# Kernel tuning notes

Measured on AMD Instinct MI355X. Metric: run time of the kernel, lower is better.

## Reference

```python
import jax, jax.numpy as jnp
import numpy as np

ETA = 3.0
KCAP = 96
POS_W = 1.2
LAMBDA_CD = 1.0
LAMBDA_P0 = 1.0
STRIDES = (8.0, 16.0, 32.0)


def _level_terms(pred_reg, pred_obj, pred_cls, gt, stride):
    """Vectorized per-level version of the triple python loop.
    pred_reg: [B,6,H,W], pred_obj/pred_cls: [B,1,H,W], gt: [B,Ng,3,2].
    Returns partial sums (reg, obj, cls, pos_count, neg_count)."""
    B, _, H, W = pred_obj.shape
    HW = H * W
    Ng = gt.shape[1]
    ys = (jnp.arange(H, dtype=jnp.float32) + 0.5) * stride
    xs = (jnp.arange(W, dtype=jnp.float32) + 0.5) * stride
    yy, xx = jnp.meshgrid(ys, xs, indexing='ij')
    px = xx.reshape(-1)  # [HW]
    py = yy.reshape(-1)
    P = px[None, None, :]  # [1,1,HW]
    Q = py[None, None, :]
    # triangle vertices, each [B,Ng,1] for broadcasting against HW
    Ax, Ay = gt[:, :, 0, 0:1], gt[:, :, 0, 1:2]
    Bx, By = gt[:, :, 1, 0:1], gt[:, :, 1, 1:2]
    Cx, Cy = gt[:, :, 2, 0:1], gt[:, :, 2, 1:2]

    def sgn(x1, y1, x2, y2, x3, y3):
        return (x1 - x3) * (y2 - y3) - (x2 - x3) * (y1 - y3)

    d1 = sgn(P, Q, Ax, Ay, Bx, By)
    d2 = sgn(P, Q, Bx, By, Cx, Cy)
    d3 = sgn(P, Q, Cx, Cy, Ax, Ay)
    has_neg = (d1 < 0) | (d2 < 0) | (d3 < 0)
    has_pos = (d1 > 0) | (d2 > 0) | (d3 > 0)
    inside = ~(has_neg & has_pos)  # [B,Ng,HW]

    def segd(x1, y1, x2, y2):
        vx, vy = x2 - x1, y2 - y1
        wx, wy = P - x1, Q - y1
        t = jnp.clip((wx * vx + wy * vy) / (vx * vx + vy * vy + 1e-9), 0.0, 1.0)
        dx = P - (x1 + t * vx)
        dy = Q - (y1 + t * vy)
        return jnp.sqrt(dx * dx + dy * dy + 1e-12)

    dist = jnp.minimum(segd(Ax, Ay, Bx, By),
                       jnp.minimum(segd(Bx, By, Cx, Cy), segd(Cx, Cy, Ax, Ay)))
    pos = inside | (dist <= ETA)  # [B,Ng,HW]

    # top-k cap: keep the KCAP positives with smallest boundary distance
    dmask = jnp.where(pos, dist, jnp.inf)
    negd, idx = jax.lax.top_k(-dmask, KCAP)  # [B,Ng,K]
    keep = jnp.isfinite(negd)                # finite <=> was a positive
    bi = jnp.arange(B)[:, None, None]
    gi = jnp.arange(Ng)[None, :, None]
    capped = jnp.zeros((B, Ng, HW), dtype=bool).at[bi, gi, idx].set(keep)
    m = capped.astype(jnp.float32)
    pos_count = m.sum()

    # objectness BCE-with-logits (pos_weight) over the whole map
    obj_t = capped.any(axis=1).astype(jnp.float32)  # [B,HW]
    x = pred_obj.reshape(B, HW)
    obj_loss = (POS_W * obj_t * jax.nn.softplus(-x)
                + (1.0 - obj_t) * jax.nn.softplus(x)).sum()
    neg_count = jnp.float32(B * HW) - obj_t.sum()

    pred_off = pred_reg.transpose(0, 2, 3, 1).reshape(B, HW, 3, 2)
    centers = jnp.stack([px, py], axis=-1)  # [HW,2]
    gt_off = (gt[:, :, None] - centers[None, None, :, None]) / stride  # [B,Ng,HW,3,2]
    p0 = ((pred_off[:, None, :, 0] - gt_off[:, :, :, 0]) ** 2).sum(-1)  # [B,Ng,HW]
    pp = pred_off[:, None, :, 1:, :]  # [B,1,HW,2,2]
    gg = gt_off[:, :, :, 1:, :]       # [B,Ng,HW,2,2]
    d = jnp.sqrt(((pp[..., :, None, :] - gg[..., None, :, :]) ** 2).sum(-1))  # [B,Ng,HW,2,2]
    cd = d.min(-1).sum(-1) + d.min(-2).sum(-1)  # [B,Ng,HW]
    reg = (m * (LAMBDA_P0 * p0 + LAMBDA_CD * cd)).sum()

    # class BCE on positives only, target = 1
    cls = (m * jax.nn.softplus(-pred_cls.reshape(B, 1, HW))).sum()
    return reg, obj_loss, cls, pos_count, neg_count


def setup_inputs() -> dict:
    key = jax.random.key(0)
    ks = jax.random.split(key, 10)
    B, Ng = 16, 32
    shapes = [(128, 128), (64, 64), (32, 32)]
    inp = {}
    i = 0
    for l, (H, W) in enumerate(shapes):
        inp[f'pred_reg{l}'] = jax.random.normal(ks[i], (B, 6, H, W), dtype=jnp.float32); i += 1
        inp[f'pred_obj{l}'] = jax.random.normal(ks[i], (B, 1, H, W), dtype=jnp.float32); i += 1
        inp[f'pred_cls{l}'] = jax.random.normal(ks[i], (B, 1, H, W), dtype=jnp.float32); i += 1
    inp['gt'] = jax.random.uniform(ks[9], (B, Ng, 3, 2), dtype=jnp.float32) * 1024.0
    return inp


def reference(pred_reg0, pred_obj0, pred_cls0,
              pred_reg1, pred_obj1, pred_cls1,
              pred_reg2, pred_obj2, pred_cls2, gt):
    levels = [(pred_reg0, pred_obj0, pred_cls0),
              (pred_reg1, pred_obj1, pred_cls1),
              (pred_reg2, pred_obj2, pred_cls2)]
    reg = obj = cls = pc = nc = jnp.float32(0.0)
    for (pr, po, pcls), s in zip(levels, STRIDES):
        r, o, c, p, n = _level_terms(pr, po, pcls, gt, s)
        reg += r; obj += o; cls += c; pc += p; nc += n
    pos_eps = jnp.maximum(pc, 1.0)
    total = (reg / pos_eps
             + obj / (pos_eps + jnp.maximum(nc, 1.0))
             + cls / pos_eps)
    return total
```

## Files before the change

kernel.cpp:

```cpp
#include <hip/hip_runtime.h>

#define KCAP 96u
#define CAP 6144
#define PBLK 512
#define NTOT 344064
#define NPAIR 1536
#define CELLS_PB 224

__device__ __forceinline__ float softplus_f(float x) {
    return fmaxf(x, 0.0f) + log1pf(expf(-fabsf(x)));
}

__device__ __forceinline__ void tri_pos_dist(
    float px, float py,
    float ax, float ay, float bx, float by, float cx, float cy,
    bool& pos, float& dist)
{
#pragma clang fp contract(off)
    float d1 = (px - bx) * (ay - by) - (ax - bx) * (py - by);
    float d2 = (px - cx) * (by - cy) - (bx - cx) * (py - cy);
    float d3 = (px - ax) * (cy - ay) - (cx - ax) * (py - ay);
    bool has_neg = (d1 < 0.f) | (d2 < 0.f) | (d3 < 0.f);
    bool has_pos = (d1 > 0.f) | (d2 > 0.f) | (d3 > 0.f);
    bool inside = !(has_neg && has_pos);

    float dAB, dBC, dCA;
    {
        float vx = bx - ax, vy = by - ay, wx = px - ax, wy = py - ay;
        float t = (wx*vx + wy*vy) / (vx*vx + vy*vy + 1e-9f);
        t = fminf(fmaxf(t, 0.0f), 1.0f);
        float dx = px - (ax + t*vx), dy = py - (ay + t*vy);
        dAB = sqrtf(dx*dx + dy*dy + 1e-12f);
    }
    {
        float vx = cx - bx, vy = cy - by, wx = px - bx, wy = py - by;
        float t = (wx*vx + wy*vy) / (vx*vx + vy*vy + 1e-9f);
        t = fminf(fmaxf(t, 0.0f), 1.0f);
        float dx = px - (bx + t*vx), dy = py - (by + t*vy);
        dBC = sqrtf(dx*dx + dy*dy + 1e-12f);
    }
    {
        float vx = ax - cx, vy = ay - cy, wx = px - cx, wy = py - cy;
        float t = (wx*vx + wy*vy) / (vx*vx + vy*vy + 1e-9f);
        t = fminf(fmaxf(t, 0.0f), 1.0f);
        float dx = px - (cx + t*vx), dy = py - (cy + t*vy);
        dCA = sqrtf(dx*dx + dy*dy + 1e-12f);
    }
    dist = fminf(dAB, fminf(dBC, dCA));
    pos = inside || (dist <= 3.0f);
}

__device__ __forceinline__ unsigned bbox_cells(const float* gp, int level) {
    int W; float stride;
    if (level == 0)      { W = 128; stride = 8.0f;  }
    else if (level == 1) { W = 64;  stride = 16.0f; }
    else                 { W = 32;  stride = 32.0f; }
    const float inv = 1.0f / stride;
    float ax = gp[0], ay = gp[1], bx = gp[2], by = gp[3], cx = gp[4], cy = gp[5];
    float minx = fminf(ax, fminf(bx, cx)), maxx = fmaxf(ax, fmaxf(bx, cx));
    float miny = fminf(ay, fminf(by, cy)), maxy = fmaxf(ay, fmaxf(by, cy));
    int wlo = max(0,     (int)floorf((minx - 3.0f) * inv - 0.5f) - 1);
    int whi = min(W - 1, (int)ceilf ((maxx + 3.0f) * inv - 0.5f) + 1);
    int hlo = max(0,     (int)floorf((miny - 3.0f) * inv - 0.5f) - 1);
    int hhi = min(W - 1, (int)ceilf ((maxy + 3.0f) * inv - 0.5f) + 1);
    int ncols = max(0, whi - wlo + 1);
    int nrows = hhi - hlo + 1;
    return (nrows > 0) ? (unsigned)(nrows * ncols) : 0u;
}

__global__ __launch_bounds__(1024) void schedule_kernel(
    const float* __restrict__ gt,
    unsigned* __restrict__ objbits,
    unsigned short* __restrict__ perm)
{
    const int t = threadIdx.x;
    for (int i = t; i < 10752; i += 1024) objbits[i] = 0u;

    __shared__ unsigned d[2048];
    #pragma unroll
    for (int s = 0; s < 2; ++s) {
        int i = t + s * 1024;
        unsigned packed = 0u;
        if (i < NPAIR) {
            unsigned nb = bbox_cells(gt + (i & 511) * 6, i >> 9);
            packed = (nb << 11) | (unsigned)i;
        }
        d[i] = packed;
    }
    __syncthreads();
    for (unsigned k = 2; k <= 2048u; k <<= 1) {
        for (unsigned j = k >> 1; j > 0; j >>= 1) {
            #pragma unroll
            for (int s = 0; s < 2; ++s) {
                int i = t + s * 1024;
                int ixj = i ^ (int)j;
                if (ixj > i) {
                    unsigned a = d[i], b = d[ixj];
                    bool desc = ((i & k) == 0);
                    if (desc ? (a < b) : (a > b)) { d[i] = b; d[ixj] = a; }
                }
            }
            __syncthreads();
        }
    }
    #pragma unroll
    for (int s = 0; s < 2; ++s) {
        int i = t + s * 1024;
        if (i < NPAIR) perm[i] = (unsigned short)(d[i] & 0x7FFu);
    }
}

__global__ __launch_bounds__(PBLK) void pair_kernel(
    const float* __restrict__ gt,
    const float* __restrict__ reg0, const float* __restrict__ cls0, const float* __restrict__ o0,
    const float* __restrict__ reg1, const float* __restrict__ cls1, const float* __restrict__ o1,
    const float* __restrict__ reg2, const float* __restrict__ cls2, const float* __restrict__ o2,
    const unsigned short* __restrict__ perm,
    unsigned* __restrict__ objbits,
    double* __restrict__ p_reg, double* __restrict__ p_cls,
    double* __restrict__ p_obj, unsigned* __restrict__ p_tc,
    unsigned* __restrict__ p_pos)
{
    const int pid = (int)perm[blockIdx.x];
    const int tid = threadIdx.x;
    const int lane = tid & 63;

    const int level = pid >> 9;
    const int pair = pid & 511;
    const int b = pair >> 5;

    int W, HW, shift, objbase;
    float stride;
    const float* pr; const float* pcl; const float* po;
    if (level == 0)      { W = 128; HW = 16384; shift = 7; stride = 8.0f;  objbase = 0;     pr = reg0; pcl = cls0; po = o0; }
    else if (level == 1) { W = 64;  HW = 4096;  shift = 6; stride = 16.0f; objbase = 8192;  pr = reg1; pcl = cls1; po = o1; }
    else                 { W = 32;  HW = 1024;  shift = 5; stride = 32.0f; objbase = 10240; pr = reg2; pcl = cls2; po = o2; }
    const int wmask = W - 1;

    double objAcc = 0.0;
    if (tid < CELLS_PB) {
        int idx = pid * CELLS_PB + tid;
        const float* o; int li;
        if (idx < 262144)      { o = o0; li = idx; }
        else if (idx < 327680) { o = o1; li = idx - 262144; }
        else                   { o = o2; li = idx - 327680; }
        objAcc = (double)softplus_f(o[li]);
    }

    const float* gp = gt + pair * 6;
    const float ax = gp[0], ay = gp[1];
    const float bx = gp[2], by = gp[3];
    const float cx = gp[4], cy = gp[5];

    const float inv = 1.0f / stride;
    float minx = fminf(ax, fminf(bx, cx)), maxx = fmaxf(ax, fmaxf(bx, cx));
    float miny = fminf(ay, fminf(by, cy)), maxy = fmaxf(ay, fmaxf(by, cy));
    int wlo = max(0,     (int)floorf((minx - 3.0f) * inv - 0.5f) - 1);
    int whi = min(W - 1, (int)ceilf ((maxx + 3.0f) * inv - 0.5f) + 1);
    int hlo = max(0,     (int)floorf((miny - 3.0f) * inv - 0.5f) - 1);
    int hhi = min(W - 1, (int)ceilf ((maxy + 3.0f) * inv - 0.5f) + 1);
    const int ncols = max(0, whi - wlo + 1);
    const int nb = (hhi - hlo + 1 > 0) ? (hhi - hlo + 1) * ncols : 0;
    const int nbR = (nb + PBLK - 1) & ~(PBLK - 1);
    const unsigned long long dmul =
        (ncols > 0) ? ((1ull << 40) / (unsigned)ncols + 1ull) : 0ull;

    __shared__ unsigned hist[2048];
    __shared__ unsigned chunk[256];
    __shared__ unsigned chunk4[64];
    __shared__ unsigned s_bits[CAP];
    __shared__ unsigned short s_hw[CAP];
    __shared__ unsigned s_cnt, s_T, s_k, s_tiecnt;
    __shared__ double red_reg[8], red_cls[8], red_obj[8];
    __shared__ unsigned red_tc[8], red_pos[8];
    unsigned* tie_hw = hist;

    if (tid == 0) { s_cnt = 0u; s_tiecnt = 0u; }
    for (int j = tid; j < 2048; j += PBLK) hist[j] = 0u;
    __syncthreads();

    auto kth_scan = [&](unsigned kk) {
        __syncthreads();
        if (tid < 256) {
            unsigned s = 0; int base = tid * 8;
            #pragma unroll
            for (int j = 0; j < 8; ++j) s += hist[base + j];
            chunk[tid] = s;
        }
        __syncthreads();
        if (tid < 64) {
            int b4 = tid * 4;
            chunk4[tid] = chunk[b4] + chunk[b4+1] + chunk[b4+2] + chunk[b4+3];
        }
        __syncthreads();
        if (tid == 0) {
            unsigned cum = 0; int t4 = 0;
            while (cum + chunk4[t4] < kk) { cum += chunk4[t4]; ++t4; }
            int t = t4 * 4;
            while (cum + chunk[t] < kk) { cum += chunk[t]; ++t; }
            int bb = t * 8;
            while (cum + hist[bb] < kk) { cum += hist[bb]; ++bb; }
            s_T = (unsigned)bb;
            s_k = kk - cum;
        }
        __syncthreads();
    };

    for (int i = tid; i < nbR; i += PBLK) {
        bool pos = false; unsigned bits = 0u; int hw = 0;
        if (i < nb) {
            int q = (int)(((unsigned long long)(unsigned)i * dmul) >> 40);
            int w = wlo + (i - q * ncols);
            int h = hlo + q;
            hw = (h << shift) | w;
            float px = (w + 0.5f) * stride;
            float py = (h + 0.5f) * stride;
            float dist;
            tri_pos_dist(px, py, ax, ay, bx, by, cx, cy, pos, dist);
            if (pos) { bits = __float_as_uint(dist); atomicAdd(&hist[bits >> 21], 1u); }
        }
        unsigned long long m = __ballot(pos);
        if (m) {
            int leader = __ffsll(m) - 1;
            unsigned base = 0u;
            if (lane == leader) base = atomicAdd(&s_cnt, (unsigned)__popcll(m));
            base = __shfl(base, leader);
            if (pos) {
                unsigned slot = base + (unsigned)__popcll(m & ((1ull << lane) - 1ull));
                if (slot < CAP) { s_bits[slot] = bits; s_hw[slot] = (unsigned short)hw; }
            }
        }
    }
    __syncthreads();

    const unsigned total = s_cnt;
    const bool fullsel = (total <= KCAP);
    unsigned n = min(total, (unsigned)CAP);
    unsigned kth_bits = 0u, tie_need = 0u;
    bool radix_fb = false;

    if (!fullsel) {
        kth_scan(KCAP);
        const unsigned T = s_T, kk1 = s_k;

        if (total > CAP) {
            if (tid == 0) s_cnt = 0u;
            __syncthreads();
            for (int i = tid; i < nbR; i += PBLK) {
                bool keep = false; unsigned bits = 0u; int hw = 0;
                if (i < nb) {
                    int q = (int)(((unsigned long long)(unsigned)i * dmul) >> 40);
                    int w = wlo + (i - q * ncols);
                    int h = hlo + q;
                    hw = (h << shift) | w;
                    float px = (w + 0.5f) * stride;
                    float py = (h + 0.5f) * stride;
                    bool pos; float dist;
                    tri_pos_dist(px, py, ax, ay, bx, by, cx, cy, pos, dist);
                    if (pos) {
                        bits = __float_as_uint(dist);
                        keep = ((bits >> 21) <= T);
                    }
                }
                unsigned long long m = __ballot(keep);
                if (m) {
                    int leader = __ffsll(m) - 1;
                    unsigned base = 0u;
                    if (lane == leader) base = atomicAdd(&s_cnt, (unsigned)__popcll(m));
                    base = __shfl(base, leader);
                    if (keep) {
                        unsigned slot = base + (unsigned)__popcll(m & ((1ull << lane) - 1ull));
                        if (slot < CAP) { s_bits[slot] = bits; s_hw[slot] = (unsigned short)hw; }
                    }
                }
            }
            __syncthreads();
            n = s_cnt;
            if (n > CAP) { radix_fb = true; }
        }

        if (!radix_fb) {
            __syncthreads();
            for (int j = tid; j < 2048; j += PBLK) hist[j] = 0u;
            __syncthreads();
            for (unsigned i = tid; i < n; i += PBLK) {
                unsigned bi = s_bits[i];
                if ((bi >> 21) == T) atomicAdd(&hist[(bi >> 10) & 0x7FFu], 1u);
            }
            kth_scan(kk1);
            unsigned prefix = (T << 11) | s_T;
            unsigned kk2 = s_k;
            __syncthreads();
            for (int j = tid; j < 2048; j += PBLK) hist[j] = 0u;
            __syncthreads();
            for (unsigned i = tid; i < n; i += PBLK) {
                unsigned bi = s_bits[i];
                if ((bi >> 10) == prefix) atomicAdd(&hist[bi & 0x3FFu], 1u);
            }
            kth_scan(kk2);
            kth_bits = (prefix << 10) | s_T;
            tie_need = s_k;
        }
    }

    double regAcc = 0.0, clsAcc = 0.0;
    unsigned tcAcc = 0u, posAcc = 0u;

    auto contribute = [&](int hw) {
        int h = hw >> shift, w = hw & wmask;
        float px = (w + 0.5f) * stride;
        float py = (h + 0.5f) * stride;
        const float* base = pr + (size_t)b * 6 * HW + hw;
        float p0x = base[0],          p0y = base[HW];
        float p1x = base[2 * HW],     p1y = base[3 * HW];
        float p2x = base[4 * HW],     p2y = base[5 * HW];
        float g0x = (ax - px) * inv,  g0y = (ay - py) * inv;
        float g1x = (bx - px) * inv,  g1y = (by - py) * inv;
        float g2x = (cx - px) * inv,  g2y = (cy - py) * inv;
        float dx0 = p0x - g0x, dy0 = p0y - g0y;
        float p0t = dx0 * dx0 + dy0 * dy0;
        float e11x = p1x - g1x, e11y = p1y - g1y;
        float e12x = p1x - g2x, e12y = p1y - g2y;
        float e21x = p2x - g1x, e21y = p2y - g1y;
        float e22x = p2x - g2x, e22y = p2y - g2y;
        float d11 = sqrtf(e11x * e11x + e11y * e11y);
        float d12 = sqrtf(e12x * e12x + e12y * e12y);
        float d21 = sqrtf(e21x * e21x + e21y * e21y);
        float d22 = sqrtf(e22x * e22x + e22y * e22y);
        float cd = fminf(d11, d12) + fminf(d21, d22) + fminf(d11, d21) + fminf(d12, d22);
        regAcc += (double)(p0t + cd);
        clsAcc += (double)softplus_f(-pcl[(size_t)b * HW + hw]);
        posAcc += 1u;

        unsigned bi = (unsigned)(b * HW + hw);
        unsigned bit = 1u << (bi & 31u);
        unsigned old = atomicOr(&objbits[objbase + (bi >> 5)], bit);
        if (!(old & bit)) {
            float x = po[(size_t)b * HW + hw];
            objAcc += (double)(1.2f * softplus_f(-x)) - (double)softplus_f(x);
            tcAcc += 1u;
        }
    };

    if (fullsel) {
        for (unsigned i = tid; i < n; i += PBLK) contribute((int)s_hw[i]);
    } else if (!radix_fb) {
        for (unsigned i = tid; i < n; i += PBLK) {
            unsigned bi = s_bits[i];
            if (bi < kth_bits) {
                contribute((int)s_hw[i]);
            } else if (bi == kth_bits) {
                unsigned t = atomicAdd(&s_tiecnt, 1u);
                if (t < 2048u) tie_hw[t] = s_hw[i];
            }
        }
        __syncthreads();
        unsigned tn = min(s_tiecnt, 2048u);
        for (unsigned i = tid; i < tn; i += PBLK) {
            unsigned hwv = tie_hw[i], rank = 0;
            for (unsigned j = 0; j < tn; ++j) rank += (tie_hw[j] < hwv) ? 1u : 0u;
            if (rank < tie_need) contribute((int)hwv);
        }
    } else {
        unsigned prefix = s_T;
        for (int p = 1; p < 3; ++p) {
            unsigned kk = s_k;
            __syncthreads();
            for (int j = tid; j < 2048; j += PBLK) hist[j] = 0u;
            __syncthreads();
            for (int i = tid; i < nb; i += PBLK) {
                int q = (int)(((unsigned long long)(unsigned)i * dmul) >> 40);
                int w = wlo + (i - q * ncols);
                int h = hlo + q;
                float px = (w + 0.5f) * stride;
                float py = (h + 0.5f) * stride;
                bool pos; float dist;
                tri_pos_dist(px, py, ax, ay, bx, by, cx, cy, pos, dist);
                if (!pos) continue;
                unsigned bits = __float_as_uint(dist);
                unsigned bin;
                if (p == 1) { if ((bits >> 21) != prefix) continue; bin = (bits >> 10) & 0x7FFu; }
                else        { if ((bits >> 10) != prefix) continue; bin = bits & 0x3FFu; }
                atomicAdd(&hist[bin], 1u);
            }
            kth_scan(kk);
            prefix = (p == 1) ? ((prefix << 11) | s_T) : ((prefix << 10) | s_T);
        }
        const unsigned kth = prefix, need = s_k;
        for (int i = tid; i < nb; i += PBLK) {
            int q = (int)(((unsigned long long)(unsigned)i * dmul) >> 40);
            int w = wlo + (i - q * ncols);
            int h = hlo + q;
            int hw = (h << shift) | w;
            float px = (w + 0.5f) * stride;
            float py = (h + 0.5f) * stride;
            bool pos; float dist;
            tri_pos_dist(px, py, ax, ay, bx, by, cx, cy, pos, dist);
            if (!pos) continue;
            unsigned bits = __float_as_uint(dist);
            if (bits < kth) {
                contribute(hw);
            } else if (bits == kth) {
                unsigned t = atomicAdd(&s_tiecnt, 1u);
                if (t < 2048u) tie_hw[t] = (unsigned)hw;
            }
        }
        __syncthreads();
        unsigned tn = min(s_tiecnt, 2048u);
        for (unsigned i = tid; i < tn; i += PBLK) {
            unsigned hwv = tie_hw[i], rank = 0;
            for (unsigned j = 0; j < tn; ++j) rank += (tie_hw[j] < hwv) ? 1u : 0u;
            if (rank < need) contribute((int)hwv);
        }
    }

    for (int off = 32; off > 0; off >>= 1) {
        regAcc += __shfl_down(regAcc, off);
        clsAcc += __shfl_down(clsAcc, off);
        objAcc += __shfl_down(objAcc, off);
        tcAcc  += __shfl_down(tcAcc, off);
        posAcc += __shfl_down(posAcc, off);
    }
    int wave = tid >> 6;
    if (lane == 0) {
        red_reg[wave] = regAcc; red_cls[wave] = clsAcc; red_obj[wave] = objAcc;
        red_tc[wave] = tcAcc; red_pos[wave] = posAcc;
    }
    __syncthreads();
    if (tid == 0) {
        double rs = 0.0, cs = 0.0, os = 0.0; unsigned ts = 0u, ps = 0u;
        #pragma unroll
        for (int i = 0; i < 8; ++i) {
            rs += red_reg[i]; cs += red_cls[i]; os += red_obj[i];
            ts += red_tc[i]; ps += red_pos[i];
        }
        p_reg[pid] = rs;
        p_cls[pid] = cs;
        p_obj[pid] = os;
        p_tc[pid]  = ts;
        p_pos[pid] = ps;
    }
}

__global__ __launch_bounds__(1024) void finalize_kernel(
    const double* __restrict__ p_reg, const double* __restrict__ p_cls,
    const double* __restrict__ p_obj, const unsigned* __restrict__ p_tc,
    const unsigned* __restrict__ p_pos,
    float* __restrict__ out)
{
    const int tid = threadIdx.x;
    double reg = 0.0, cls = 0.0, obj = 0.0;
    unsigned pc = 0u, tc = 0u;
    for (int i = tid; i < NPAIR; i += 1024) {
        reg += p_reg[i]; cls += p_cls[i]; obj += p_obj[i];
        tc += p_tc[i]; pc += p_pos[i];
    }
    for (int off = 32; off > 0; off >>= 1) {
        reg += __shfl_down(reg, off);
        cls += __shfl_down(cls, off);
        obj += __shfl_down(obj, off);
        pc  += __shfl_down(pc, off);
        tc  += __shfl_down(tc, off);
    }
    __shared__ double rr[16], rc[16], ro[16];
    __shared__ unsigned rp[16], rn[16];
    int wave = tid >> 6, lane = tid & 63;
    if (lane == 0) { rr[wave] = reg; rc[wave] = cls; ro[wave] = obj; rp[wave] = pc; rn[wave] = tc; }
    __syncthreads();
    if (tid == 0) {
        double sreg = 0, scls = 0, sobj = 0; unsigned spc = 0, stc = 0;
        #pragma unroll
        for (int i = 0; i < 16; ++i) {
            sreg += rr[i]; scls += rc[i]; sobj += ro[i]; spc += rp[i]; stc += rn[i];
        }
        double nc = (double)NTOT - (double)stc;
        double pos_eps = fmax((double)spc, 1.0);
        double den = pos_eps + fmax(nc, 1.0);
        out[0] = (float)(sreg / pos_eps + sobj / den + scls / pos_eps);
    }
}

extern "C" void kernel_launch(void* const* d_in, const int* in_sizes, int n_in,
                              void* d_out, int out_size, void* d_ws, size_t ws_size,
                              hipStream_t stream)
{
    (void)in_sizes; (void)n_in; (void)out_size; (void)ws_size;
    const float* reg0 = (const float*)d_in[0];
    const float* obj0 = (const float*)d_in[1];
    const float* cls0 = (const float*)d_in[2];
    const float* reg1 = (const float*)d_in[3];
    const float* obj1 = (const float*)d_in[4];
    const float* cls1 = (const float*)d_in[5];
    const float* reg2 = (const float*)d_in[6];
    const float* obj2 = (const float*)d_in[7];
    const float* cls2 = (const float*)d_in[8];
    const float* gt   = (const float*)d_in[9];

    char* ws = (char*)d_ws;
    unsigned*       objbits = (unsigned*)ws;
    double*         p_reg   = (double*)(ws + 43008);
    double*         p_cls   = (double*)(ws + 55296);
    double*         p_obj   = (double*)(ws + 67584);
    unsigned*       p_tc    = (unsigned*)(ws + 79872);
    unsigned*       p_pos   = (unsigned*)(ws + 86016);
    unsigned short* perm    = (unsigned short*)(ws + 92160);

    schedule_kernel<<<1, 1024, 0, stream>>>(gt, objbits, perm);
    pair_kernel<<<NPAIR, PBLK, 0, stream>>>(gt,
                                            reg0, cls0, obj0,
                                            reg1, cls1, obj1,
                                            reg2, cls2, obj2,
                                            perm, objbits,
                                            p_reg, p_cls, p_obj, p_tc, p_pos);
    finalize_kernel<<<1, 1024, 0, stream>>>(p_reg, p_cls, p_obj, p_tc, p_pos,
                                            (float*)d_out);
}
```

Measured before the change: 160.1 us.

## Clip per-row cell spans to triangle half-planes and bucket-sort pairs by estimated work

```diff
diff --git a/kernel.cpp b/kernel.cpp
--- a/kernel.cpp
+++ b/kernel.cpp
@@ -50,24 +50,6 @@
     pos = inside || (dist <= 3.0f);
 }
 
-__device__ __forceinline__ unsigned bbox_cells(const float* gp, int level) {
-    int W; float stride;
-    if (level == 0)      { W = 128; stride = 8.0f;  }
-    else if (level == 1) { W = 64;  stride = 16.0f; }
-    else                 { W = 32;  stride = 32.0f; }
-    const float inv = 1.0f / stride;
-    float ax = gp[0], ay = gp[1], bx = gp[2], by = gp[3], cx = gp[4], cy = gp[5];
-    float minx = fminf(ax, fminf(bx, cx)), maxx = fmaxf(ax, fmaxf(bx, cx));
-    float miny = fminf(ay, fminf(by, cy)), maxy = fmaxf(ay, fmaxf(by, cy));
-    int wlo = max(0,     (int)floorf((minx - 3.0f) * inv - 0.5f) - 1);
-    int whi = min(W - 1, (int)ceilf ((maxx + 3.0f) * inv - 0.5f) + 1);
-    int hlo = max(0,     (int)floorf((miny - 3.0f) * inv - 0.5f) - 1);
-    int hhi = min(W - 1, (int)ceilf ((maxy + 3.0f) * inv - 0.5f) + 1);
-    int ncols = max(0, whi - wlo + 1);
-    int nrows = hhi - hlo + 1;
-    return (nrows > 0) ? (unsigned)(nrows * ncols) : 0u;
-}
-
 __global__ __launch_bounds__(1024) void schedule_kernel(
     const float* __restrict__ gt,
     unsigned* __restrict__ objbits,
@@ -76,37 +58,45 @@
     const int t = threadIdx.x;
     for (int i = t; i < 10752; i += 1024) objbits[i] = 0u;
 
-    __shared__ unsigned d[2048];
+    __shared__ unsigned cnt[128];
+    __shared__ unsigned start[128];
+    if (t < 128) cnt[t] = 0u;
+    __syncthreads();
+
+    unsigned bkt[2] = {0u, 0u};
     #pragma unroll
     for (int s = 0; s < 2; ++s) {
         int i = t + s * 1024;
-        unsigned packed = 0u;
         if (i < NPAIR) {
-            unsigned nb = bbox_cells(gt + (i & 511) * 6, i >> 9);
-            packed = (nb << 11) | (unsigned)i;
-        }
-        d[i] = packed;
-    }
-    __syncthreads();
-    for (unsigned k = 2; k <= 2048u; k <<= 1) {
-        for (unsigned j = k >> 1; j > 0; j >>= 1) {
-            #pragma unroll
-            for (int s = 0; s < 2; ++s) {
-                int i = t + s * 1024;
-                int ixj = i ^ (int)j;
-                if (ixj > i) {
-                    unsigned a = d[i], b = d[ixj];
-                    bool desc = ((i & k) == 0);
-                    if (desc ? (a < b) : (a > b)) { d[i] = b; d[ixj] = a; }
-                }
-            }
-            __syncthreads();
-        }
-    }
+            const float* gp = gt + (i & 511) * 6;
+            float ax = gp[0], ay = gp[1], bx = gp[2], by = gp[3], cx = gp[4], cy = gp[5];
+            float stride = (i >> 9) == 0 ? 8.0f : ((i >> 9) == 1 ? 16.0f : 32.0f);
+            float inv = 1.0f / stride;
+            float area2 = fabsf((bx - ax) * (cy - ay) - (cx - ax) * (by - ay));
+            float l1 = sqrtf((ax-bx)*(ax-bx) + (ay-by)*(ay-by));
+            float l2 = sqrtf((bx-cx)*(bx-cx) + (by-cy)*(by-cy));
+            float l3 = sqrtf((cx-ax)*(cx-ax) + (cy-ay)*(cy-ay));
+            float est = 0.5f * area2 * inv * inv + 3.05f * inv * (l1 + l2 + l3) + 40.0f;
+            unsigned b = min(127u, (unsigned)est >> 7);
+            bkt[s] = b;
+            atomicAdd(&cnt[b], 1u);
+        }
+    }
+    __syncthreads();
+    if (t == 0) {
+        unsigned acc = 0u;
+        for (int b = 127; b >= 0; --b) { start[b] = acc; acc += cnt[b]; }
+    }
+    __syncthreads();
+    if (t < 128) cnt[t] = 0u;
+    __syncthreads();
     #pragma unroll
     for (int s = 0; s < 2; ++s) {
         int i = t + s * 1024;
-        if (i < NPAIR) perm[i] = (unsigned short)(d[i] & 0x7FFu);
+        if (i < NPAIR) {
+            unsigned slot = start[bkt[s]] + atomicAdd(&cnt[bkt[s]], 1u);
+            perm[slot] = (unsigned short)i;
+        }
     }
 }
 
@@ -159,25 +149,81 @@
     int whi = min(W - 1, (int)ceilf ((maxx + 3.0f) * inv - 0.5f) + 1);
     int hlo = max(0,     (int)floorf((miny - 3.0f) * inv - 0.5f) - 1);
     int hhi = min(W - 1, (int)ceilf ((maxy + 3.0f) * inv - 0.5f) + 1);
-    const int ncols = max(0, whi - wlo + 1);
-    const int nb = (hhi - hlo + 1 > 0) ? (hhi - hlo + 1) * ncols : 0;
-    const int nbR = (nb + PBLK - 1) & ~(PBLK - 1);
-    const unsigned long long dmul =
-        (ncols > 0) ? ((1ull << 40) / (unsigned)ncols + 1ull) : 0ull;
+    const int nrows = max(0, hhi - hlo + 1);
+
+    float area2 = (bx - ax) * (cy - ay) - (cx - ax) * (by - ay);
+    const float sgnf = (area2 > 0.f) ? 1.f : ((area2 < 0.f) ? -1.f : 0.f);
+    const float a1 = ay - by, a2 = by - cy, a3 = cy - ay;
+    const float T1 = 3.05f * sqrtf((ax-bx)*(ax-bx) + (ay-by)*(ay-by));
+    const float T2 = 3.05f * sqrtf((bx-cx)*(bx-cx) + (by-cy)*(by-cy));
+    const float T3 = 3.05f * sqrtf((cx-ax)*(cx-ax) + (cy-ay)*(cy-ay));
 
     __shared__ unsigned hist[2048];
     __shared__ unsigned chunk[256];
     __shared__ unsigned chunk4[64];
     __shared__ unsigned s_bits[CAP];
     __shared__ unsigned short s_hw[CAP];
+    __shared__ short s_rowlo[128];
+    __shared__ unsigned s_rowstart[129];
     __shared__ unsigned s_cnt, s_T, s_k, s_tiecnt;
     __shared__ double red_reg[8], red_cls[8], red_obj[8];
     __shared__ unsigned red_tc[8], red_pos[8];
     unsigned* tie_hw = hist;
 
-    if (tid == 0) { s_cnt = 0u; s_tiecnt = 0u; }
+    if (tid == 0) { s_cnt = 0u; s_tiecnt = 0u; s_rowstart[0] = 0u; }
     for (int j = tid; j < 2048; j += PBLK) hist[j] = 0u;
-    __syncthreads();
+
+    if (tid < nrows) {
+        float py = ((hlo + tid) + 0.5f) * stride;
+        int wl = wlo, wh = whi;
+        if (sgnf != 0.f) {
+            float xlo = minx - 3.0f - stride;
+            float xhi = maxx + 3.0f + stride;
+            bool ok = true;
+            float c1 = -bx * a1 - (ax - bx) * (py - by);
+            float c2 = -cx * a2 - (bx - cx) * (py - cy);
+            float c3 = -ax * a3 - (cx - ax) * (py - ay);
+            float ap, cp;
+            ap = sgnf * a1; cp = sgnf * c1;
+            if (ap > 0.f)      xlo = fmaxf(xlo, (-T1 - cp) / ap);
+            else if (ap < 0.f) xhi = fminf(xhi, (-T1 - cp) / ap);
+            else if (cp < -T1) ok = false;
+            ap = sgnf * a2; cp = sgnf * c2;
+            if (ap > 0.f)      xlo = fmaxf(xlo, (-T2 - cp) / ap);
+            else if (ap < 0.f) xhi = fminf(xhi, (-T2 - cp) / ap);
+            else if (cp < -T2) ok = false;
+            ap = sgnf * a3; cp = sgnf * c3;
+            if (ap > 0.f)      xlo = fmaxf(xlo, (-T3 - cp) / ap);
+            else if (ap < 0.f) xhi = fminf(xhi, (-T3 - cp) / ap);
+            else if (cp < -T3) ok = false;
+            if (ok) {
+                wl = max(wlo, (int)floorf(xlo * inv - 0.5f) - 1);
+                wh = min(whi, (int)ceilf (xhi * inv - 0.5f) + 1);
+            } else { wl = 1; wh = 0; }
+        }
+        s_rowlo[tid] = (short)wl;
+        s_rowstart[tid + 1] = (wh >= wl) ? (unsigned)(wh - wl + 1) : 0u;
+    }
+    __syncthreads();
+    if (tid == 0)
+        for (int r = 0; r < nrows; ++r) s_rowstart[r + 1] += s_rowstart[r];
+    __syncthreads();
+
+    const int M  = (nrows > 0) ? (int)s_rowstart[nrows] : 0;
+    const int MR = (M + PBLK - 1) & ~(PBLK - 1);
+
+    auto map_cell = [&](int j, int& hw, float& px, float& py) {
+        int lo = 0, hi = nrows - 1;
+        while (lo < hi) {
+            int mid = (lo + hi + 1) >> 1;
+            if (s_rowstart[mid] <= (unsigned)j) lo = mid; else hi = mid - 1;
+        }
+        int w = (int)s_rowlo[lo] + (j - (int)s_rowstart[lo]);
+        int h = hlo + lo;
+        hw = (h << shift) | w;
+        px = (w + 0.5f) * stride;
+        py = (h + 0.5f) * stride;
+    };
 
     auto kth_scan = [&](unsigned kk) {
         __syncthreads();
@@ -206,15 +252,11 @@
         __syncthreads();
     };
 
-    for (int i = tid; i < nbR; i += PBLK) {
+    for (int i = tid; i < MR; i += PBLK) {
         bool pos = false; unsigned bits = 0u; int hw = 0;
-        if (i < nb) {
-            int q = (int)(((unsigned long long)(unsigned)i * dmul) >> 40);
-            int w = wlo + (i - q * ncols);
-            int h = hlo + q;
-            hw = (h << shift) | w;
-            float px = (w + 0.5f) * stride;
-            float py = (h + 0.5f) * stride;
+        if (i < M) {
+            float px, py;
+            map_cell(i, hw, px, py);
             float dist;
             tri_pos_dist(px, py, ax, ay, bx, by, cx, cy, pos, dist);
             if (pos) { bits = __float_as_uint(dist); atomicAdd(&hist[bits >> 21], 1u); }
@@ -246,15 +288,11 @@
         if (total > CAP) {
             if (tid == 0) s_cnt = 0u;
             __syncthreads();
-            for (int i = tid; i < nbR; i += PBLK) {
+            for (int i = tid; i < MR; i += PBLK) {
                 bool keep = false; unsigned bits = 0u; int hw = 0;
-                if (i < nb) {
-                    int q = (int)(((unsigned long long)(unsigned)i * dmul) >> 40);
-                    int w = wlo + (i - q * ncols);
-                    int h = hlo + q;
-                    hw = (h << shift) | w;
-                    float px = (w + 0.5f) * stride;
-                    float py = (h + 0.5f) * stride;
+                if (i < M) {
+                    float px, py;
+                    map_cell(i, hw, px, py);
                     bool pos; float dist;
                     tri_pos_dist(px, py, ax, ay, bx, by, cx, cy, pos, dist);
                     if (pos) {
@@ -368,12 +406,9 @@
             __syncthreads();
             for (int j = tid; j < 2048; j += PBLK) hist[j] = 0u;
             __syncthreads();
-            for (int i = tid; i < nb; i += PBLK) {
-                int q = (int)(((unsigned long long)(unsigned)i * dmul) >> 40);
-                int w = wlo + (i - q * ncols);
-                int h = hlo + q;
-                float px = (w + 0.5f) * stride;
-                float py = (h + 0.5f) * stride;
+            for (int i = tid; i < M; i += PBLK) {
+                int hw; float px, py;
+                map_cell(i, hw, px, py);
                 bool pos; float dist;
                 tri_pos_dist(px, py, ax, ay, bx, by, cx, cy, pos, dist);
                 if (!pos) continue;
@@ -387,13 +422,9 @@
             prefix = (p == 1) ? ((prefix << 11) | s_T) : ((prefix << 10) | s_T);
         }
         const unsigned kth = prefix, need = s_k;
-        for (int i = tid; i < nb; i += PBLK) {
-            int q = (int)(((unsigned long long)(unsigned)i * dmul) >> 40);
-            int w = wlo + (i - q * ncols);
-            int h = hlo + q;
-            int hw = (h << shift) | w;
-            float px = (w + 0.5f) * stride;
-            float py = (h + 0.5f) * stride;
+        for (int i = tid; i < M; i += PBLK) {
+            int hw; float px, py;
+            map_cell(i, hw, px, py);
             bool pos; float dist;
             tri_pos_dist(px, py, ax, ay, bx, by, cx, cy, pos, dist);
             if (!pos) continue;
```

Result: faster. 138.7 us (-13.4%).
